# Kernel tuning notes

Measured on AMD Instinct MI355X. Metric: run time of the kernel, lower is better.

The kernel has to match this reference:

```python
import jax, jax.numpy as jnp
from jax import lax
import numpy as np

B, T, NCLS, D = 64, 2048, 20, 2048
LCS_LEN, FSD_LEN = 64, 32
LAMB1, LAMB2, LAMB3 = 1.0, 5e-5, 8e-5
LAMB_LCS, LAMB_FSD = 0.01, 0.01
FEAT_MARGIN = 50.0
THRES = 0.5
GAMMA = 0.1


def cos_sim(a, b):
    a = a / jnp.linalg.norm(a, axis=1, keepdims=True)
    b = b / jnp.linalg.norm(b, axis=1, keepdims=True)
    return a @ b.T


def dp_fsd(c0, c1):
    # soft-LCS/DTW-style recurrence with maxGamma (soft max) over 3 neighbors
    h = c0.shape[-1] // 2
    m = cos_sim(c0[:, :h], c1[:, :h])  # [L, L]
    g = cos_sim(c0[:, h:], c1[:, h:])  # [L, L]
    L = m.shape[0]

    def row_step(prev_row, mg):
        m_row, g_row = mg
        diag = prev_row[:-1]  # C[i-1, j-1]
        up = prev_row[1:]     # C[i-1, j]

        def col_step(left, xs):  # left = C[i, j-1]
            d, u, mij, gij = xs
            neigh = jnp.stack([d, gij + u, gij + left])
            val = mij + GAMMA * jax.nn.logsumexp(neigh / GAMMA)
            return val, val

        _, row_vals = lax.scan(col_step, jnp.zeros((), m.dtype), (diag, up, m_row, g_row))
        new_row = jnp.concatenate([jnp.zeros((1,), m.dtype), row_vals])
        return new_row, None

    final_row, _ = lax.scan(row_step, jnp.zeros(L + 1, m.dtype), (m, g))
    return final_row[-1]


def dp_lcs(c0, c1):
    s = cos_sim(c0, c1)  # [L, L]
    L = s.shape[0]

    def row_step(prev_row, s_row):
        diag = prev_row[:-1]
        up = prev_row[1:]

        def col_step(left, xs):
            d, u, sij = xs
            val = jnp.where(sij > THRES, d + sij, jnp.maximum(u, left))
            return val, val

        _, row_vals = lax.scan(col_step, jnp.zeros((), s.dtype), (diag, up, s_row))
        return jnp.concatenate([jnp.zeros((1,), s.dtype), row_vals]), None

    final_row, _ = lax.scan(row_step, jnp.zeros(L + 1, s.dtype), s)
    return final_row[-1]


def cls_criterion(p, lab):
    return -jnp.mean(jnp.sum(jnp.log(p + 1e-10) * lab, axis=1))


def forward_once(ai_cls, ac_cls, ab_cls, vlab, att, ai_feat, ac_feat, ab_feat, ai_cas):
    bs = ai_cls.shape[0]
    ones = jnp.ones((bs, 1), ai_cls.dtype)
    zeros = jnp.zeros((bs, 1), ai_cls.dtype)
    inst_lab = jnp.concatenate([vlab, zeros], axis=1)
    cont_lab = jnp.concatenate([vlab, ones], axis=1)
    back_lab = jnp.concatenate([jnp.zeros_like(vlab), ones], axis=1)
    inst_lab = inst_lab / jnp.sum(inst_lab, axis=1, keepdims=True)
    cont_lab = cont_lab / jnp.sum(cont_lab, axis=1, keepdims=True)
    back_lab = back_lab / jnp.sum(back_lab, axis=1, keepdims=True)

    inst_loss = cls_criterion(ai_cls, inst_lab)
    cont_loss = cls_criterion(ac_cls, cont_lab)
    back_loss = cls_criterion(ab_cls, back_lab)

    guide_loss = jnp.mean(jnp.sum(jnp.abs(1.0 - ai_cas[:, :, -1] - lax.stop_gradient(att[:, :, 0])), axis=1))

    n_inst = jnp.linalg.norm(ai_feat, axis=1)
    n_cont = jnp.linalg.norm(ac_feat, axis=1)
    n_back = jnp.linalg.norm(ab_feat, axis=1)
    f1 = jnp.maximum(FEAT_MARGIN - n_inst + n_cont, 0.0)
    f2 = jnp.maximum(FEAT_MARGIN - n_cont + n_back, 0.0)
    f3 = n_back
    feat_loss = jnp.mean((f1 + f2 + f3) ** 2)

    sparse_loss = jnp.mean(jnp.sum(att[:, :, :2], axis=1))

    cls_loss = inst_loss + cont_loss + back_loss  # THUMOS14 weights 1/1/1
    return cls_loss + LAMB1 * guide_loss + LAMB2 * feat_loss + LAMB3 * sparse_loss


def _pair_loss(vals, pair_label):
    bs = vals.shape[0]
    pos = jnp.sum(vals * pair_label)
    neg = jnp.sum(vals * (1.0 - pair_label))
    pos_num = jnp.sum(pair_label)
    neg_num = bs - pos_num
    return neg / (neg_num + 1e-10) - pos / (pos_num + 1e-10)


def ftcl_forward(act_inst_cls_0, act_cont_cls_0, act_back_cls_0, vid_label_0, temp_att_0,
                 act_inst_feat_0, act_cont_feat_0, act_back_feat_0, act_inst_cas_0,
                 lcs_candi_0, fsd_act_candi_0, fsd_bak_candi_0,
                 act_inst_cls_1, act_cont_cls_1, act_back_cls_1, vid_label_1, temp_att_1,
                 act_inst_feat_1, act_cont_feat_1, act_back_feat_1, act_inst_cas_1,
                 lcs_candi_1, fsd_act_candi_1, fsd_bak_candi_1):
    loss_0 = forward_once(act_inst_cls_0, act_cont_cls_0, act_back_cls_0, vid_label_0, temp_att_0,
                          act_inst_feat_0, act_cont_feat_0, act_back_feat_0, act_inst_cas_0)
    loss_1 = forward_once(act_inst_cls_1, act_cont_cls_1, act_back_cls_1, vid_label_1, temp_att_1,
                          act_inst_feat_1, act_cont_feat_1, act_back_feat_1, act_inst_cas_1)
    acm_loss = (loss_0 + loss_1) / 2.0

    pair_label = (jnp.sum(vid_label_0 * vid_label_1, axis=1) > 0).astype(jnp.float32)  # [B]

    lcs = jax.vmap(dp_lcs)(lcs_candi_0, lcs_candi_1)  # [B]
    lcs_loss = _pair_loss(lcs, pair_label)

    # pair==1 -> act_1, pair==0 -> bak_1 (matches the per-sample branch in torch)
    fsd_c1 = jnp.where(pair_label[:, None, None] > 0, fsd_act_candi_1, fsd_bak_candi_1)
    fsd = jax.vmap(dp_fsd)(fsd_act_candi_0, fsd_c1)  # [B]
    fsd_loss = _pair_loss(fsd, pair_label)

    return acm_loss + LAMB_LCS * lcs_loss + LAMB_FSD * fsd_loss


def setup_inputs() -> dict:
    key = jax.random.key(0)
    ks = iter(jax.random.split(key, 32))
    rand = lambda s: jax.random.uniform(next(ks), s, jnp.float32)
    randn = lambda s: jax.random.normal(next(ks), s, jnp.float32)
    inp = {}
    for sfx in ('0', '1'):
        inp[f'act_inst_cls_{sfx}'] = rand((B, NCLS + 1))
        inp[f'act_cont_cls_{sfx}'] = rand((B, NCLS + 1))
        inp[f'act_back_cls_{sfx}'] = rand((B, NCLS + 1))
        inp[f'vid_label_{sfx}'] = jnp.ones((B, NCLS), jnp.float32)
        inp[f'temp_att_{sfx}'] = rand((B, T, 3))
        inp[f'act_inst_feat_{sfx}'] = randn((B, D))
        inp[f'act_cont_feat_{sfx}'] = randn((B, D))
        inp[f'act_back_feat_{sfx}'] = randn((B, D))
        inp[f'act_inst_cas_{sfx}'] = rand((B, T, NCLS + 1))
        inp[f'lcs_candi_{sfx}'] = randn((B, LCS_LEN, D))
        inp[f'fsd_act_candi_{sfx}'] = randn((B, FSD_LEN, D))
        inp[f'fsd_bak_candi_{sfx}'] = randn((B, FSD_LEN, D))
    return inp


def reference(act_inst_cls_0, act_cont_cls_0, act_back_cls_0, vid_label_0, temp_att_0,
              act_inst_feat_0, act_cont_feat_0, act_back_feat_0, act_inst_cas_0,
              lcs_candi_0, fsd_act_candi_0, fsd_bak_candi_0,
              act_inst_cls_1, act_cont_cls_1, act_back_cls_1, vid_label_1, temp_att_1,
              act_inst_feat_1, act_cont_feat_1, act_back_feat_1, act_inst_cas_1,
              lcs_candi_1, fsd_act_candi_1, fsd_bak_candi_1):
    return ftcl_forward(act_inst_cls_0, act_cont_cls_0, act_back_cls_0, vid_label_0, temp_att_0,
                        act_inst_feat_0, act_cont_feat_0, act_back_feat_0, act_inst_cas_0,
                        lcs_candi_0, fsd_act_candi_0, fsd_bak_candi_0,
                        act_inst_cls_1, act_cont_cls_1, act_back_cls_1, vid_label_1, temp_att_1,
                        act_inst_feat_1, act_cont_feat_1, act_back_feat_1, act_inst_cas_1,
                        lcs_candi_1, fsd_act_candi_1, fsd_bak_candi_1)
```

## Files before the change

### kernel.cpp

```cpp
#include <hip/hip_runtime.h>
#include <math.h>

#define Bn 64
#define Tn 2048
#define NCLS 20
#define Dn 2048
#define LCSL 64
#define FSDL 32

typedef __bf16 bf16x4 __attribute__((ext_vector_type(4)));
typedef __bf16 bf16x8 __attribute__((ext_vector_type(8)));
typedef float f32x4 __attribute__((ext_vector_type(4)));

#define WS_LCS 0
#define WS_FSD 64
#define WS_NORM 128
#define WS_GS 512
template <int NS>
struct WsOff {
    static constexpr size_t LSQ = 1024;
    static constexpr size_t FSQ = LSQ + (size_t)64 * NS * 128;
    static constexpr size_t SPART = FSQ + (size_t)64 * NS * 64;
    static constexpr size_t MG = SPART + (size_t)64 * NS * 4096;
    static constexpr size_t SC = MG + (size_t)64 * NS * 1024;
    static constexpr size_t PL = SC + 16;
    static constexpr size_t END = PL + 64;
};

#define AUXB 224

template <int NS>
__global__ __launch_bounds__(256) void mega_kernel(
    const float* __restrict__ lcs0, const float* __restrict__ lcs1,
    const float* __restrict__ fA0, const float* __restrict__ fA1,
    const float* __restrict__ fB1,
    const float* __restrict__ vid0, const float* __restrict__ vid1,
    const float* __restrict__ cas0, const float* __restrict__ att0,
    const float* __restrict__ cas1, const float* __restrict__ att1,
    const float* __restrict__ f0, const float* __restrict__ f1,
    const float* __restrict__ f2, const float* __restrict__ f3,
    const float* __restrict__ f4, const float* __restrict__ f5,
    float* __restrict__ ws) {
    constexpr int L = (NS == 16) ? 4 : 3;
    constexpr int KC = 2048 / NS / 64;
    using O = WsOff<NS>;
    __shared__ __align__(16) __bf16 tA[2][4096];
    __shared__ __align__(16) __bf16 tB[2][4096];
    const int t = threadIdx.x;
    const int bid = blockIdx.x;
    const int w = t >> 6, lane = t & 63;
    const int quad = lane >> 4, l16 = lane & 15;

    if (bid < 128) {
        const int gb = bid;
        const int N = Bn * Tn;
        float g0 = 0.f, s0 = 0.f, g1 = 0.f, s1 = 0.f;
        for (int n = gb * 256 + t; n < 2 * N; n += 128 * 256) {
            int sfx = (n >= N);
            int m = sfx ? (n - N) : n;
            const float* cas = sfx ? cas1 : cas0;
            const float* att = sfx ? att1 : att0;
            float a0 = att[m * 3 + 0];
            float a1 = att[m * 3 + 1];
            float g = fabsf(1.0f - cas[m * (NCLS + 1) + NCLS] - a0);
            float s = a0 + a1;
            if (sfx) { g1 += g; s1 += s; } else { g0 += g; s0 += s; }
        }
        float* red = (float*)tA;
        float vals[4] = {g0, s0, g1, s1};
        #pragma unroll
        for (int v = 0; v < 4; ++v) red[v * 256 + t] = vals[v];
        __syncthreads();
        for (int o = 128; o; o >>= 1) {
            if (t < o) {
                #pragma unroll
                for (int v = 0; v < 4; ++v) red[v * 256 + t] += red[v * 256 + t + o];
            }
            __syncthreads();
        }
        if (t < 4) ws[WS_GS + gb * 4 + t] = red[t * 256];
    } else if (bid < AUXB) {
        int R = (bid - 128) * 4 + w;
        const float* arr[6] = {f0, f1, f2, f3, f4, f5};
        const float* p = arr[R >> 6] + (size_t)(R & 63) * Dn;
        float s = 0.f;
        #pragma unroll
        for (int qd = 0; qd < 8; ++qd) {
            float4 v = *(const float4*)(p + qd * 256 + lane * 4);
            s += v.x * v.x + v.y * v.y + v.z * v.z + v.w * v.w;
        }
        for (int off = 32; off; off >>= 1) s += __shfl_down(s, off);
        if (lane == 0) ws[WS_NORM + R] = sqrtf(s);
    } else if (bid < AUXB + 64 * NS) {
        const int gb = bid - AUXB;
        const int b = gb >> L, ks = gb & (NS - 1);
        const float* c0 = lcs0 + (size_t)b * LCSL * Dn + ks * (2048 / NS);
        const float* c1 = lcs1 + (size_t)b * LCSL * Dn + ks * (2048 / NS);

        f32x4 acc[4] = {};
        float sqa[4] = {0.f, 0.f, 0.f, 0.f}, sqb[4] = {0.f, 0.f, 0.f, 0.f};
        float4 pA[4], pB[4];

        auto LOADL = [&](int st) {
            #pragma unroll
            for (int l = 0; l < 4; ++l) {
                int idx4 = l * 256 + t;
                int row = idx4 >> 4, kq4 = idx4 & 15;
                pA[l] = *(const float4*)(c0 + (size_t)row * Dn + st * 64 + kq4 * 4);
                pB[l] = *(const float4*)(c1 + (size_t)row * Dn + st * 64 + kq4 * 4);
            }
        };
        auto WRITEL = [&](int buf) {
            #pragma unroll
            for (int l = 0; l < 4; ++l) {
                int idx4 = l * 256 + t;
                int row = idx4 >> 4, kq4 = idx4 & 15;
                int c = kq4 >> 1, h = kq4 & 1;
                int pos = row * 64 + ((c ^ (row & 7)) << 3) + h * 4;
                float4 av = pA[l], bv = pB[l];
                bf16x4 a4 = {(__bf16)av.x, (__bf16)av.y, (__bf16)av.z, (__bf16)av.w};
                bf16x4 b4 = {(__bf16)bv.x, (__bf16)bv.y, (__bf16)bv.z, (__bf16)bv.w};
                *(bf16x4*)&tA[buf][pos] = a4;
                *(bf16x4*)&tB[buf][pos] = b4;
                sqa[l] += av.x * av.x + av.y * av.y + av.z * av.z + av.w * av.w;
                sqb[l] += bv.x * bv.x + bv.y * bv.y + bv.z * bv.z + bv.w * bv.w;
            }
        };

        LOADL(0);
        WRITEL(0);
        if (KC > 1) LOADL(1);
        __syncthreads();
        for (int kc = 0; kc < KC; ++kc) {
            const int cur = kc & 1;
            #pragma unroll
            for (int s = 0; s < 2; ++s) {
                int ar = w * 16 + l16;
                int ac_ = (s * 4 + quad) ^ (ar & 7);
                bf16x8 af = *(const bf16x8*)&tA[cur][ar * 64 + (ac_ << 3)];
                #pragma unroll
                for (int tj = 0; tj < 4; ++tj) {
                    int br = tj * 16 + l16;
                    int bc = (s * 4 + quad) ^ (br & 7);
                    bf16x8 bf = *(const bf16x8*)&tB[cur][br * 64 + (bc << 3)];
                    acc[tj] = __builtin_amdgcn_mfma_f32_16x16x32_bf16(af, bf, acc[tj], 0, 0, 0);
                }
            }
            if (kc + 1 < KC) {
                WRITEL(cur ^ 1);
                if (kc + 2 < KC) LOADL(kc + 2);
                __syncthreads();
            }
        }
        float* dst = ws + O::SPART + (size_t)(b * NS + ks) * 4096;
        #pragma unroll
        for (int tj = 0; tj < 4; ++tj)
            #pragma unroll
            for (int rg = 0; rg < 4; ++rg)
                dst[(w * 16 + quad * 4 + rg) * 64 + tj * 16 + l16] = acc[tj][rg];
        #pragma unroll
        for (int l = 0; l < 4; ++l) {
            float sa = sqa[l], sb = sqb[l];
            #pragma unroll
            for (int m = 1; m < 16; m <<= 1) {
                sa += __shfl_xor(sa, m);
                sb += __shfl_xor(sb, m);
            }
            if ((t & 15) == 0) {
                int r = l * 16 + (t >> 4);
                float* q = ws + O::LSQ + (size_t)(b * NS + ks) * 128;
                q[r] = sa;
                q[64 + r] = sb;
            }
        }
    } else {
        const int qb = bid - AUXB - 64 * NS;
        const int b = qb >> L;
        const int idx = qb & (NS - 1);
        const int half = idx >> (L - 1);
        const int ks = idx & (NS / 2 - 1);
        float ps = 0.f;
        for (int c = 0; c < NCLS; ++c) ps += vid0[b * NCLS + c] * vid1[b * NCLS + c];
        const float* base1 = (ps > 0.f) ? fA1 : fB1;
        const float* c0 = fA0 + (size_t)b * FSDL * Dn + half * 1024 + ks * (2048 / NS);
        const float* c1 = base1 + (size_t)b * FSDL * Dn + half * 1024 + ks * (2048 / NS);
        const int wi = w >> 1, wj = w & 1;

        f32x4 acc = {};
        float sqa[2] = {0.f, 0.f}, sqb[2] = {0.f, 0.f};
        float4 pA[2], pB[2];

        auto LOADF = [&](int st) {
            #pragma unroll
            for (int l = 0; l < 2; ++l) {
                int idx4 = l * 256 + t;
                int row = idx4 >> 4, kq4 = idx4 & 15;
                pA[l] = *(const float4*)(c0 + (size_t)row * Dn + st * 64 + kq4 * 4);
                pB[l] = *(const float4*)(c1 + (size_t)row * Dn + st * 64 + kq4 * 4);
            }
        };
        auto WRITEF = [&](int buf) {
            #pragma unroll
            for (int l = 0; l < 2; ++l) {
                int idx4 = l * 256 + t;
                int row = idx4 >> 4, kq4 = idx4 & 15;
                int c = kq4 >> 1, h = kq4 & 1;
                int pos = row * 64 + ((c ^ (row & 7)) << 3) + h * 4;
                float4 av = pA[l], bv = pB[l];
                bf16x4 a4 = {(__bf16)av.x, (__bf16)av.y, (__bf16)av.z, (__bf16)av.w};
                bf16x4 b4 = {(__bf16)bv.x, (__bf16)bv.y, (__bf16)bv.z, (__bf16)bv.w};
                *(bf16x4*)&tA[buf][pos] = a4;
                *(bf16x4*)&tB[buf][pos] = b4;
                sqa[l] += av.x * av.x + av.y * av.y + av.z * av.z + av.w * av.w;
                sqb[l] += bv.x * bv.x + bv.y * bv.y + bv.z * bv.z + bv.w * bv.w;
            }
        };

        LOADF(0);
        WRITEF(0);
        if (KC > 1) LOADF(1);
        __syncthreads();
        for (int kc = 0; kc < KC; ++kc) {
            const int cur = kc & 1;
            #pragma unroll
            for (int s = 0; s < 2; ++s) {
                int ar = wi * 16 + l16;
                int ac_ = (s * 4 + quad) ^ (ar & 7);
                bf16x8 af = *(const bf16x8*)&tA[cur][ar * 64 + (ac_ << 3)];
                int br = wj * 16 + l16;
                int bc = (s * 4 + quad) ^ (br & 7);
                bf16x8 bf = *(const bf16x8*)&tB[cur][br * 64 + (bc << 3)];
                acc = __builtin_amdgcn_mfma_f32_16x16x32_bf16(af, bf, acc, 0, 0, 0);
            }
            if (kc + 1 < KC) {
                WRITEF(cur ^ 1);
                if (kc + 2 < KC) LOADF(kc + 2);
                __syncthreads();
            }
        }
        float* dst = ws + O::MG + (size_t)((b * 2 + half) * (NS / 2) + ks) * 1024;
        #pragma unroll
        for (int rg = 0; rg < 4; ++rg)
            dst[(wi * 16 + quad * 4 + rg) * 32 + wj * 16 + l16] = acc[rg];
        #pragma unroll
        for (int l = 0; l < 2; ++l) {
            float sa = sqa[l], sb = sqb[l];
            #pragma unroll
            for (int m = 1; m < 16; m <<= 1) {
                sa += __shfl_xor(sa, m);
                sb += __shfl_xor(sb, m);
            }
            if ((t & 15) == 0) {
                int r = l * 16 + (t >> 4);
                float* qq = ws + O::FSQ + (size_t)((b * 2 + half) * (NS / 2) + ks) * 64;
                qq[r] = sa;
                qq[32 + r] = sb;
            }
        }
    }
}

__device__ __forceinline__ float4 wbr4(float4 v, float4* redw, int t) {
    #pragma unroll
    for (int m = 1; m < 64; m <<= 1) {
        v.x += __shfl_xor(v.x, m);
        v.y += __shfl_xor(v.y, m);
        v.z += __shfl_xor(v.z, m);
        v.w += __shfl_xor(v.w, m);
    }
    if ((t & 63) == 0) redw[t >> 6] = v;
    __syncthreads();
    float4 r;
    r.x = redw[0].x + redw[1].x + redw[2].x + redw[3].x;
    r.y = redw[0].y + redw[1].y + redw[2].y + redw[3].y;
    r.z = redw[0].z + redw[1].z + redw[2].z + redw[3].z;
    r.w = redw[0].w + redw[1].w + redw[2].w + redw[3].w;
    __syncthreads();
    return r;
}

template <int NS>
__global__ __launch_bounds__(256) void dp_kernel(
    float* __restrict__ ws,
    const float* __restrict__ ai0, const float* __restrict__ ac0,
    const float* __restrict__ ab0, const float* __restrict__ vid0,
    const float* __restrict__ ai1, const float* __restrict__ ac1,
    const float* __restrict__ ab1, const float* __restrict__ vid1) {
    using O = WsOff<NS>;
    const int t = threadIdx.x;
    if (blockIdx.x < 64) {
        const int b = blockIdx.x;
        __shared__ float S[64 * 68];
        __shared__ float inv[128];
        if (t < 128) {
            float s = 0.f;
            #pragma unroll
            for (int ks = 0; ks < NS; ++ks)
                s += ws[O::LSQ + (size_t)(b * NS + ks) * 128 + t];
            inv[t] = 1.0f / sqrtf(s);
        }
        __syncthreads();
        const float* sp = ws + O::SPART + (size_t)b * NS * 4096;
        #pragma unroll
        for (int qd = 0; qd < 4; ++qd) {
            int idx4 = qd * 256 + t;
            int i = idx4 >> 4, j = (idx4 & 15) * 4;
            float4 v = {0.f, 0.f, 0.f, 0.f};
            #pragma unroll
            for (int ks = 0; ks < NS; ++ks) {
                float4 p = *(const float4*)(sp + (size_t)ks * 4096 + idx4 * 4);
                v.x += p.x; v.y += p.y; v.z += p.z; v.w += p.w;
            }
            float ri = inv[i];
            S[i * 68 + j + 0] = v.x * ri * inv[64 + j + 0];
            S[i * 68 + j + 1] = v.y * ri * inv[64 + j + 1];
            S[i * 68 + j + 2] = v.z * ri * inv[64 + j + 2];
            S[i * 68 + j + 3] = v.w * ri * inv[64 + j + 3];
        }
        __syncthreads();
        if (t < 64) {
            float prev = 0.f, prevprev = 0.f;
            float sval_next = S[t * 68 + 0];
            for (int d = 2; d <= 128; ++d) {
                float s = sval_next;
                int jn = d - t - 1;
                if (jn >= 0 && jn < 64) sval_next = S[t * 68 + jn];
                float up = __shfl_up(prev, 1);
                float dg = __shfl_up(prevprev, 1);
                if (t == 0) { up = 0.f; dg = 0.f; }
                int j = d - t - 1;
                float left = prev;
                float val = (s > 0.5f) ? (dg + s) : fmaxf(up, left);
                float cur = (j >= 1 && j <= 64) ? val : 0.f;
                prevprev = prev;
                prev = cur;
            }
            if (t == 63) ws[WS_LCS + b] = prev;
        }
    } else if (blockIdx.x < 128) {
        const int b = blockIdx.x - 64;
        __shared__ float M[32 * 36], G[32 * 36];
        __shared__ float inv[128];
        if (t < 128) {
            int half = t >> 6, sub = t & 63;
            float s = 0.f;
            #pragma unroll
            for (int ks = 0; ks < NS / 2; ++ks)
                s += ws[O::FSQ + (size_t)((b * 2 + half) * (NS / 2) + ks) * 64 + sub];
            inv[t] = 1.0f / sqrtf(s);
        }
        __syncthreads();
        {
            int idx4 = t;
            int i = idx4 >> 3, j = (idx4 & 7) * 4;
            float4 vM = {0.f, 0.f, 0.f, 0.f}, vG = {0.f, 0.f, 0.f, 0.f};
            #pragma unroll
            for (int ks = 0; ks < NS / 2; ++ks) {
                float4 pM = *(const float4*)(ws + O::MG + (size_t)((b * 2 + 0) * (NS / 2) + ks) * 1024 + idx4 * 4);
                float4 pG = *(const float4*)(ws + O::MG + (size_t)((b * 2 + 1) * (NS / 2) + ks) * 1024 + idx4 * 4);
                vM.x += pM.x; vM.y += pM.y; vM.z += pM.z; vM.w += pM.w;
                vG.x += pG.x; vG.y += pG.y; vG.z += pG.z; vG.w += pG.w;
            }
            float riM = inv[i], riG = inv[64 + i];
            M[i * 36 + j + 0] = vM.x * riM * inv[32 + j + 0];
            M[i * 36 + j + 1] = vM.y * riM * inv[32 + j + 1];
            M[i * 36 + j + 2] = vM.z * riM * inv[32 + j + 2];
            M[i * 36 + j + 3] = vM.w * riM * inv[32 + j + 3];
            G[i * 36 + j + 0] = vG.x * riG * inv[96 + j + 0];
            G[i * 36 + j + 1] = vG.y * riG * inv[96 + j + 1];
            G[i * 36 + j + 2] = vG.z * riG * inv[96 + j + 2];
            G[i * 36 + j + 3] = vG.w * riG * inv[96 + j + 3];
        }
        __syncthreads();
        if (t < 32) {
            float prev = 0.f, prevprev = 0.f;
            float m_next = M[t * 36 + 0], g_next = G[t * 36 + 0];
            for (int d = 2; d <= 64; ++d) {
                float m = m_next, g = g_next;
                int jn = d - t - 1;
                if (jn >= 0 && jn < 32) { m_next = M[t * 36 + jn]; g_next = G[t * 36 + jn]; }
                float up = __shfl_up(prev, 1);
                float dg = __shfl_up(prevprev, 1);
                if (t == 0) { up = 0.f; dg = 0.f; }
                int j = d - t - 1;
                float left = prev;
                float x0 = dg * 10.0f;
                float x1 = (g + up) * 10.0f;
                float x2 = (g + left) * 10.0f;
                float mx = fmaxf(x0, fmaxf(x1, x2));
                float lse = mx + __logf(__expf(x0 - mx) + __expf(x1 - mx) + __expf(x2 - mx));
                float val = m + 0.1f * lse;
                float cur = (j >= 1 && j <= 32) ? val : 0.f;
                prevprev = prev;
                prev = cur;
            }
            if (t == 31) ws[WS_FSD + b] = prev;
        }
    } else if (blockIdx.x == 128) {
        __shared__ float rs0[Bn], rs1[Bn];
        __shared__ __align__(16) float4 redw[4];
        float plreg = 0.f;
        if (t < Bn) {
            float s0 = 0.f, s1 = 0.f, pp = 0.f;
            for (int c = 0; c < NCLS; ++c) {
                float a = vid0[t * NCLS + c], bl = vid1[t * NCLS + c];
                s0 += a; s1 += bl; pp += a * bl;
            }
            rs0[t] = s0;
            rs1[t] = s1;
            plreg = (pp > 0.f) ? 1.f : 0.f;
            ws[O::PL + t] = plreg;
        }
        __syncthreads();
        float inst0 = 0.f, cont0 = 0.f, back0 = 0.f;
        float inst1 = 0.f, cont1 = 0.f, back1 = 0.f;
        for (int idx = t; idx < Bn * (NCLS + 1); idx += 256) {
            int b = idx / (NCLS + 1), c = idx % (NCLS + 1);
            float v0 = (c < NCLS) ? vid0[b * NCLS + c] : 0.f;
            float v1 = (c < NCLS) ? vid1[b * NCLS + c] : 0.f;
            float wI0 = (c < NCLS) ? (v0 / rs0[b]) : 0.f;
            float wC0 = ((c < NCLS) ? v0 : 1.f) / (rs0[b] + 1.f);
            float wI1 = (c < NCLS) ? (v1 / rs1[b]) : 0.f;
            float wC1 = ((c < NCLS) ? v1 : 1.f) / (rs1[b] + 1.f);
            inst0 += logf(ai0[idx] + 1e-10f) * wI0;
            cont0 += logf(ac0[idx] + 1e-10f) * wC0;
            inst1 += logf(ai1[idx] + 1e-10f) * wI1;
            cont1 += logf(ac1[idx] + 1e-10f) * wC1;
            if (c == NCLS) {
                back0 += logf(ab0[idx] + 1e-10f);
                back1 += logf(ab1[idx] + 1e-10f);
            }
        }
        float4 r1 = wbr4({inst0, cont0, back0, inst1}, redw, t);
        float4 r2 = wbr4({cont1, back1, plreg, 0.f}, redw, t);
        if (t == 0) {
            ws[O::SC + 0] = r1.x; ws[O::SC + 1] = r1.y; ws[O::SC + 2] = r1.z;
            ws[O::SC + 3] = r1.w; ws[O::SC + 4] = r2.x; ws[O::SC + 5] = r2.y;
            ws[O::SC + 12] = r2.z;
        }
    } else if (blockIdx.x == 129) {
        __shared__ __align__(16) float4 redw[4];
        float4 g = {0.f, 0.f, 0.f, 0.f};
        if (t < 128) g = *(const float4*)&ws[WS_GS + t * 4];
        float4 r = wbr4(g, redw, t);
        if (t == 0) {
            ws[O::SC + 6] = r.x; ws[O::SC + 7] = r.y;
            ws[O::SC + 8] = r.z; ws[O::SC + 9] = r.w;
        }
    } else if (blockIdx.x == 130) {
        __shared__ __align__(16) float4 redw[4];
        float fv0 = 0.f, fv1 = 0.f;
        if (t < Bn) {
            const float* nm = ws + WS_NORM;
            {
                float ni = nm[0 * Bn + t], nc = nm[1 * Bn + t], nb = nm[2 * Bn + t];
                float f1 = fmaxf(50.0f - ni + nc, 0.f);
                float f2 = fmaxf(50.0f - nc + nb, 0.f);
                float f = f1 + f2 + nb;
                fv0 = f * f;
            }
            {
                float ni = nm[3 * Bn + t], nc = nm[4 * Bn + t], nb = nm[5 * Bn + t];
                float f1 = fmaxf(50.0f - ni + nc, 0.f);
                float f2 = fmaxf(50.0f - nc + nb, 0.f);
                float f = f1 + f2 + nb;
                fv1 = f * f;
            }
        }
        float4 r = wbr4({fv0, fv1, 0.f, 0.f}, redw, t);
        if (t == 0) {
            ws[O::SC + 10] = r.x; ws[O::SC + 11] = r.y;
        }
    }
}

template <int NS>
__global__ __launch_bounds__(64) void final_kernel(const float* __restrict__ ws,
                                                   float* __restrict__ out) {
    using O = WsOff<NS>;
    const int t = threadIdx.x;
    float pl = ws[O::PL + t];
    float lv = ws[WS_LCS + t];
    float fv = ws[WS_FSD + t];
    float4 v = {lv * pl, lv * (1.f - pl), fv * pl, fv * (1.f - pl)};
    #pragma unroll
    for (int m = 1; m < 64; m <<= 1) {
        v.x += __shfl_xor(v.x, m);
        v.y += __shfl_xor(v.y, m);
        v.z += __shfl_xor(v.z, m);
        v.w += __shfl_xor(v.w, m);
    }
    if (t == 0) {
        const float* sc = ws + O::SC;
        float cls0 = -(sc[0] + sc[1] + sc[2]) / (float)Bn;
        float cls1 = -(sc[3] + sc[4] + sc[5]) / (float)Bn;
        float guide0 = sc[6] / (float)Bn;
        float sparse0 = sc[7] / (float)(Bn * 2);
        float guide1 = sc[8] / (float)Bn;
        float sparse1 = sc[9] / (float)(Bn * 2);
        float sFeat0 = sc[10] / (float)Bn;
        float sFeat1 = sc[11] / (float)Bn;
        float loss0 = cls0 + 1.0f * guide0 + 5e-05f * sFeat0 + 8e-05f * sparse0;
        float loss1 = cls1 + 1.0f * guide1 + 5e-05f * sFeat1 + 8e-05f * sparse1;
        float acm = 0.5f * (loss0 + loss1);
        float posn = sc[12];
        float negn = (float)Bn - posn;
        float lcs_loss = v.y / (negn + 1e-10f) - v.x / (posn + 1e-10f);
        float fsd_loss = v.w / (negn + 1e-10f) - v.z / (posn + 1e-10f);
        out[0] = acm + 0.01f * lcs_loss + 0.01f * fsd_loss;
    }
}

extern "C" void kernel_launch(void* const* d_in, const int* in_sizes, int n_in,
                              void* d_out, int out_size, void* d_ws, size_t ws_size,
                              hipStream_t stream) {
    (void)in_sizes; (void)n_in; (void)out_size;
    const float* ai0  = (const float*)d_in[0];
    const float* ac0  = (const float*)d_in[1];
    const float* ab0  = (const float*)d_in[2];
    const float* vid0 = (const float*)d_in[3];
    const float* att0 = (const float*)d_in[4];
    const float* fi0  = (const float*)d_in[5];
    const float* fc0  = (const float*)d_in[6];
    const float* fb0  = (const float*)d_in[7];
    const float* cas0 = (const float*)d_in[8];
    const float* lcs0 = (const float*)d_in[9];
    const float* fsdA0 = (const float*)d_in[10];
    const float* ai1  = (const float*)d_in[12];
    const float* ac1  = (const float*)d_in[13];
    const float* ab1  = (const float*)d_in[14];
    const float* vid1 = (const float*)d_in[15];
    const float* att1 = (const float*)d_in[16];
    const float* fi1  = (const float*)d_in[17];
    const float* fc1  = (const float*)d_in[18];
    const float* fb1  = (const float*)d_in[19];
    const float* cas1 = (const float*)d_in[20];
    const float* lcs1 = (const float*)d_in[21];
    const float* fsdA1 = (const float*)d_in[22];
    const float* fsdB1 = (const float*)d_in[23];

    float* ws = (float*)d_ws;

    if (ws_size >= WsOff<16>::END * sizeof(float)) {
        mega_kernel<16><<<AUXB + 128 * 16, 256, 0, stream>>>(
            lcs0, lcs1, fsdA0, fsdA1, fsdB1, vid0, vid1, cas0, att0, cas1, att1,
            fi0, fc0, fb0, fi1, fc1, fb1, ws);
        dp_kernel<16><<<131, 256, 0, stream>>>(ws, ai0, ac0, ab0, vid0, ai1, ac1, ab1, vid1);
        final_kernel<16><<<1, 64, 0, stream>>>(ws, (float*)d_out);
    } else {
        mega_kernel<8><<<AUXB + 128 * 8, 256, 0, stream>>>(
            lcs0, lcs1, fsdA0, fsdA1, fsdB1, vid0, vid1, cas0, att0, cas1, att1,
            fi0, fc0, fb0, fi1, fc1, fb1, ws);
        dp_kernel<8><<<131, 256, 0, stream>>>(ws, ai0, ac0, ab0, vid0, ai1, ac1, ab1, vid1);
        final_kernel<8><<<1, 64, 0, stream>>>(ws, (float*)d_out);
    }
}
```

Before: 224.5 us.

## Fuse final reduction into DP kernel via atomic counter and move class loss into mega kernel

Moves the classification-loss block from the DP kernel into an extra block of the mega kernel. The final reduction now runs as a last block of the DP kernel, which spin-waits on an atomic counter cleared by a memset, replacing a separate final kernel launch. It also fixes the split count at 8, widens the DP kernel to 512 threads, and adds a memset call. The spin-wait depends on the waiting block being scheduled alongside the producer blocks.

```diff
diff --git a/kernel.cpp b/kernel.cpp
--- a/kernel.cpp
+++ b/kernel.cpp
@@ -24,241 +24,12 @@
     static constexpr size_t MG = SPART + (size_t)64 * NS * 4096;
     static constexpr size_t SC = MG + (size_t)64 * NS * 1024;
     static constexpr size_t PL = SC + 16;
-    static constexpr size_t END = PL + 64;
+    static constexpr size_t CNT = PL + 64;
+    static constexpr size_t END = CNT + 4;
 };
 
-#define AUXB 224
-
-template <int NS>
-__global__ __launch_bounds__(256) void mega_kernel(
-    const float* __restrict__ lcs0, const float* __restrict__ lcs1,
-    const float* __restrict__ fA0, const float* __restrict__ fA1,
-    const float* __restrict__ fB1,
-    const float* __restrict__ vid0, const float* __restrict__ vid1,
-    const float* __restrict__ cas0, const float* __restrict__ att0,
-    const float* __restrict__ cas1, const float* __restrict__ att1,
-    const float* __restrict__ f0, const float* __restrict__ f1,
-    const float* __restrict__ f2, const float* __restrict__ f3,
-    const float* __restrict__ f4, const float* __restrict__ f5,
-    float* __restrict__ ws) {
-    constexpr int L = (NS == 16) ? 4 : 3;
-    constexpr int KC = 2048 / NS / 64;
-    using O = WsOff<NS>;
-    __shared__ __align__(16) __bf16 tA[2][4096];
-    __shared__ __align__(16) __bf16 tB[2][4096];
-    const int t = threadIdx.x;
-    const int bid = blockIdx.x;
-    const int w = t >> 6, lane = t & 63;
-    const int quad = lane >> 4, l16 = lane & 15;
-
-    if (bid < 128) {
-        const int gb = bid;
-        const int N = Bn * Tn;
-        float g0 = 0.f, s0 = 0.f, g1 = 0.f, s1 = 0.f;
-        for (int n = gb * 256 + t; n < 2 * N; n += 128 * 256) {
-            int sfx = (n >= N);
-            int m = sfx ? (n - N) : n;
-            const float* cas = sfx ? cas1 : cas0;
-            const float* att = sfx ? att1 : att0;
-            float a0 = att[m * 3 + 0];
-            float a1 = att[m * 3 + 1];
-            float g = fabsf(1.0f - cas[m * (NCLS + 1) + NCLS] - a0);
-            float s = a0 + a1;
-            if (sfx) { g1 += g; s1 += s; } else { g0 += g; s0 += s; }
-        }
-        float* red = (float*)tA;
-        float vals[4] = {g0, s0, g1, s1};
-        #pragma unroll
-        for (int v = 0; v < 4; ++v) red[v * 256 + t] = vals[v];
-        __syncthreads();
-        for (int o = 128; o; o >>= 1) {
-            if (t < o) {
-                #pragma unroll
-                for (int v = 0; v < 4; ++v) red[v * 256 + t] += red[v * 256 + t + o];
-            }
-            __syncthreads();
-        }
-        if (t < 4) ws[WS_GS + gb * 4 + t] = red[t * 256];
-    } else if (bid < AUXB) {
-        int R = (bid - 128) * 4 + w;
-        const float* arr[6] = {f0, f1, f2, f3, f4, f5};
-        const float* p = arr[R >> 6] + (size_t)(R & 63) * Dn;
-        float s = 0.f;
-        #pragma unroll
-        for (int qd = 0; qd < 8; ++qd) {
-            float4 v = *(const float4*)(p + qd * 256 + lane * 4);
-            s += v.x * v.x + v.y * v.y + v.z * v.z + v.w * v.w;
-        }
-        for (int off = 32; off; off >>= 1) s += __shfl_down(s, off);
-        if (lane == 0) ws[WS_NORM + R] = sqrtf(s);
-    } else if (bid < AUXB + 64 * NS) {
-        const int gb = bid - AUXB;
-        const int b = gb >> L, ks = gb & (NS - 1);
-        const float* c0 = lcs0 + (size_t)b * LCSL * Dn + ks * (2048 / NS);
-        const float* c1 = lcs1 + (size_t)b * LCSL * Dn + ks * (2048 / NS);
-
-        f32x4 acc[4] = {};
-        float sqa[4] = {0.f, 0.f, 0.f, 0.f}, sqb[4] = {0.f, 0.f, 0.f, 0.f};
-        float4 pA[4], pB[4];
-
-        auto LOADL = [&](int st) {
-            #pragma unroll
-            for (int l = 0; l < 4; ++l) {
-                int idx4 = l * 256 + t;
-                int row = idx4 >> 4, kq4 = idx4 & 15;
-                pA[l] = *(const float4*)(c0 + (size_t)row * Dn + st * 64 + kq4 * 4);
-                pB[l] = *(const float4*)(c1 + (size_t)row * Dn + st * 64 + kq4 * 4);
-            }
-        };
-        auto WRITEL = [&](int buf) {
-            #pragma unroll
-            for (int l = 0; l < 4; ++l) {
-                int idx4 = l * 256 + t;
-                int row = idx4 >> 4, kq4 = idx4 & 15;
-                int c = kq4 >> 1, h = kq4 & 1;
-                int pos = row * 64 + ((c ^ (row & 7)) << 3) + h * 4;
-                float4 av = pA[l], bv = pB[l];
-                bf16x4 a4 = {(__bf16)av.x, (__bf16)av.y, (__bf16)av.z, (__bf16)av.w};
-                bf16x4 b4 = {(__bf16)bv.x, (__bf16)bv.y, (__bf16)bv.z, (__bf16)bv.w};
-                *(bf16x4*)&tA[buf][pos] = a4;
-                *(bf16x4*)&tB[buf][pos] = b4;
-                sqa[l] += av.x * av.x + av.y * av.y + av.z * av.z + av.w * av.w;
-                sqb[l] += bv.x * bv.x + bv.y * bv.y + bv.z * bv.z + bv.w * bv.w;
-            }
-        };
-
-        LOADL(0);
-        WRITEL(0);
-        if (KC > 1) LOADL(1);
-        __syncthreads();
-        for (int kc = 0; kc < KC; ++kc) {
-            const int cur = kc & 1;
-            #pragma unroll
-            for (int s = 0; s < 2; ++s) {
-                int ar = w * 16 + l16;
-                int ac_ = (s * 4 + quad) ^ (ar & 7);
-                bf16x8 af = *(const bf16x8*)&tA[cur][ar * 64 + (ac_ << 3)];
-                #pragma unroll
-                for (int tj = 0; tj < 4; ++tj) {
-                    int br = tj * 16 + l16;
-                    int bc = (s * 4 + quad) ^ (br & 7);
-                    bf16x8 bf = *(const bf16x8*)&tB[cur][br * 64 + (bc << 3)];
-                    acc[tj] = __builtin_amdgcn_mfma_f32_16x16x32_bf16(af, bf, acc[tj], 0, 0, 0);
-                }
-            }
-            if (kc + 1 < KC) {
-                WRITEL(cur ^ 1);
-                if (kc + 2 < KC) LOADL(kc + 2);
-                __syncthreads();
-            }
-        }
-        float* dst = ws + O::SPART + (size_t)(b * NS + ks) * 4096;
-        #pragma unroll
-        for (int tj = 0; tj < 4; ++tj)
-            #pragma unroll
-            for (int rg = 0; rg < 4; ++rg)
-                dst[(w * 16 + quad * 4 + rg) * 64 + tj * 16 + l16] = acc[tj][rg];
-        #pragma unroll
-        for (int l = 0; l < 4; ++l) {
-            float sa = sqa[l], sb = sqb[l];
-            #pragma unroll
-            for (int m = 1; m < 16; m <<= 1) {
-                sa += __shfl_xor(sa, m);
-                sb += __shfl_xor(sb, m);
-            }
-            if ((t & 15) == 0) {
-                int r = l * 16 + (t >> 4);
-                float* q = ws + O::LSQ + (size_t)(b * NS + ks) * 128;
-                q[r] = sa;
-                q[64 + r] = sb;
-            }
-        }
-    } else {
-        const int qb = bid - AUXB - 64 * NS;
-        const int b = qb >> L;
-        const int idx = qb & (NS - 1);
-        const int half = idx >> (L - 1);
-        const int ks = idx & (NS / 2 - 1);
-        float ps = 0.f;
-        for (int c = 0; c < NCLS; ++c) ps += vid0[b * NCLS + c] * vid1[b * NCLS + c];
-        const float* base1 = (ps > 0.f) ? fA1 : fB1;
-        const float* c0 = fA0 + (size_t)b * FSDL * Dn + half * 1024 + ks * (2048 / NS);
-        const float* c1 = base1 + (size_t)b * FSDL * Dn + half * 1024 + ks * (2048 / NS);
-        const int wi = w >> 1, wj = w & 1;
-
-        f32x4 acc = {};
-        float sqa[2] = {0.f, 0.f}, sqb[2] = {0.f, 0.f};
-        float4 pA[2], pB[2];
-
-        auto LOADF = [&](int st) {
-            #pragma unroll
-            for (int l = 0; l < 2; ++l) {
-                int idx4 = l * 256 + t;
-                int row = idx4 >> 4, kq4 = idx4 & 15;
-                pA[l] = *(const float4*)(c0 + (size_t)row * Dn + st * 64 + kq4 * 4);
-                pB[l] = *(const float4*)(c1 + (size_t)row * Dn + st * 64 + kq4 * 4);
-            }
-        };
-        auto WRITEF = [&](int buf) {
-            #pragma unroll
-            for (int l = 0; l < 2; ++l) {
-                int idx4 = l * 256 + t;
-                int row = idx4 >> 4, kq4 = idx4 & 15;
-                int c = kq4 >> 1, h = kq4 & 1;
-                int pos = row * 64 + ((c ^ (row & 7)) << 3) + h * 4;
-                float4 av = pA[l], bv = pB[l];
-                bf16x4 a4 = {(__bf16)av.x, (__bf16)av.y, (__bf16)av.z, (__bf16)av.w};
-                bf16x4 b4 = {(__bf16)bv.x, (__bf16)bv.y, (__bf16)bv.z, (__bf16)bv.w};
-                *(bf16x4*)&tA[buf][pos] = a4;
-                *(bf16x4*)&tB[buf][pos] = b4;
-                sqa[l] += av.x * av.x + av.y * av.y + av.z * av.z + av.w * av.w;
-                sqb[l] += bv.x * bv.x + bv.y * bv.y + bv.z * bv.z + bv.w * bv.w;
-            }
-        };
-
-        LOADF(0);
-        WRITEF(0);
-        if (KC > 1) LOADF(1);
-        __syncthreads();
-        for (int kc = 0; kc < KC; ++kc) {
-            const int cur = kc & 1;
-            #pragma unroll
-            for (int s = 0; s < 2; ++s) {
-                int ar = wi * 16 + l16;
-                int ac_ = (s * 4 + quad) ^ (ar & 7);
-                bf16x8 af = *(const bf16x8*)&tA[cur][ar * 64 + (ac_ << 3)];
-                int br = wj * 16 + l16;
-                int bc = (s * 4 + quad) ^ (br & 7);
-                bf16x8 bf = *(const bf16x8*)&tB[cur][br * 64 + (bc << 3)];
-                acc = __builtin_amdgcn_mfma_f32_16x16x32_bf16(af, bf, acc, 0, 0, 0);
-            }
-            if (kc + 1 < KC) {
-                WRITEF(cur ^ 1);
-                if (kc + 2 < KC) LOADF(kc + 2);
-                __syncthreads();
-            }
-        }
-        float* dst = ws + O::MG + (size_t)((b * 2 + half) * (NS / 2) + ks) * 1024;
-        #pragma unroll
-        for (int rg = 0; rg < 4; ++rg)
-            dst[(wi * 16 + quad * 4 + rg) * 32 + wj * 16 + l16] = acc[rg];
-        #pragma unroll
-        for (int l = 0; l < 2; ++l) {
-            float sa = sqa[l], sb = sqb[l];
-            #pragma unroll
-            for (int m = 1; m < 16; m <<= 1) {
-                sa += __shfl_xor(sa, m);
-                sb += __shfl_xor(sb, m);
-            }
-            if ((t & 15) == 0) {
-                int r = l * 16 + (t >> 4);
-                float* qq = ws + O::FSQ + (size_t)((b * 2 + half) * (NS / 2) + ks) * 64;
-                qq[r] = sa;
-                qq[32 + r] = sb;
-            }
-        }
-    }
-}
+#define NSU 8
+#define AUXB 225
 
 __device__ __forceinline__ float4 wbr4(float4 v, float4* redw, int t) {
     #pragma unroll
@@ -280,13 +51,287 @@
 }
 
 template <int NS>
-__global__ __launch_bounds__(256) void dp_kernel(
-    float* __restrict__ ws,
+__global__ __launch_bounds__(256) void mega_kernel(
+    const float* __restrict__ lcs0, const float* __restrict__ lcs1,
+    const float* __restrict__ fA0, const float* __restrict__ fA1,
+    const float* __restrict__ fB1,
+    const float* __restrict__ vid0, const float* __restrict__ vid1,
+    const float* __restrict__ cas0, const float* __restrict__ att0,
+    const float* __restrict__ cas1, const float* __restrict__ att1,
+    const float* __restrict__ f0, const float* __restrict__ f1,
+    const float* __restrict__ f2, const float* __restrict__ f3,
+    const float* __restrict__ f4, const float* __restrict__ f5,
     const float* __restrict__ ai0, const float* __restrict__ ac0,
-    const float* __restrict__ ab0, const float* __restrict__ vid0,
-    const float* __restrict__ ai1, const float* __restrict__ ac1,
-    const float* __restrict__ ab1, const float* __restrict__ vid1) {
+    const float* __restrict__ ab0, const float* __restrict__ ai1,
+    const float* __restrict__ ac1, const float* __restrict__ ab1,
+    float* __restrict__ ws) {
+    constexpr int L = (NS == 16) ? 4 : 3;
+    constexpr int KC = 2048 / NS / 64;
     using O = WsOff<NS>;
+    __shared__ __align__(16) __bf16 tA[2][4096];
+    __shared__ __align__(16) __bf16 tB[2][4096];
+    const int t = threadIdx.x;
+    const int bid = blockIdx.x;
+    const int w = t >> 6, lane = t & 63;
+    const int quad = lane >> 4, l16 = lane & 15;
+
+    if (bid < 128) {
+        const int gb = bid;
+        const int N = Bn * Tn;
+        float g0 = 0.f, s0 = 0.f, g1 = 0.f, s1 = 0.f;
+        for (int n = gb * 256 + t; n < 2 * N; n += 128 * 256) {
+            int sfx = (n >= N);
+            int m = sfx ? (n - N) : n;
+            const float* cas = sfx ? cas1 : cas0;
+            const float* att = sfx ? att1 : att0;
+            float a0 = att[m * 3 + 0];
+            float a1 = att[m * 3 + 1];
+            float g = fabsf(1.0f - cas[m * (NCLS + 1) + NCLS] - a0);
+            float s = a0 + a1;
+            if (sfx) { g1 += g; s1 += s; } else { g0 += g; s0 += s; }
+        }
+        float* red = (float*)tA;
+        float vals[4] = {g0, s0, g1, s1};
+        #pragma unroll
+        for (int v = 0; v < 4; ++v) red[v * 256 + t] = vals[v];
+        __syncthreads();
+        for (int o = 128; o; o >>= 1) {
+            if (t < o) {
+                #pragma unroll
+                for (int v = 0; v < 4; ++v) red[v * 256 + t] += red[v * 256 + t + o];
+            }
+            __syncthreads();
+        }
+        if (t < 4) ws[WS_GS + gb * 4 + t] = red[t * 256];
+    } else if (bid < 224) {
+        int R = (bid - 128) * 4 + w;
+        const float* arr[6] = {f0, f1, f2, f3, f4, f5};
+        const float* p = arr[R >> 6] + (size_t)(R & 63) * Dn;
+        float s = 0.f;
+        #pragma unroll
+        for (int qd = 0; qd < 8; ++qd) {
+            float4 v = *(const float4*)(p + qd * 256 + lane * 4);
+            s += v.x * v.x + v.y * v.y + v.z * v.z + v.w * v.w;
+        }
+        for (int off = 32; off; off >>= 1) s += __shfl_down(s, off);
+        if (lane == 0) ws[WS_NORM + R] = sqrtf(s);
+    } else if (bid < AUXB) {
+        float* rs0 = (float*)tA;
+        float* rs1 = (float*)tA + 64;
+        float4* redw = (float4*)tB;
+        float plreg = 0.f;
+        if (t < Bn) {
+            float s0 = 0.f, s1 = 0.f, pp = 0.f;
+            for (int c = 0; c < NCLS; ++c) {
+                float a = vid0[t * NCLS + c], bl = vid1[t * NCLS + c];
+                s0 += a; s1 += bl; pp += a * bl;
+            }
+            rs0[t] = s0;
+            rs1[t] = s1;
+            plreg = (pp > 0.f) ? 1.f : 0.f;
+            ws[O::PL + t] = plreg;
+        }
+        __syncthreads();
+        float inst0 = 0.f, cont0 = 0.f, back0 = 0.f;
+        float inst1 = 0.f, cont1 = 0.f, back1 = 0.f;
+        for (int idx = t; idx < Bn * (NCLS + 1); idx += 256) {
+            int b = idx / (NCLS + 1), c = idx % (NCLS + 1);
+            float v0 = (c < NCLS) ? vid0[b * NCLS + c] : 0.f;
+            float v1 = (c < NCLS) ? vid1[b * NCLS + c] : 0.f;
+            float wI0 = (c < NCLS) ? (v0 / rs0[b]) : 0.f;
+            float wC0 = ((c < NCLS) ? v0 : 1.f) / (rs0[b] + 1.f);
+            float wI1 = (c < NCLS) ? (v1 / rs1[b]) : 0.f;
+            float wC1 = ((c < NCLS) ? v1 : 1.f) / (rs1[b] + 1.f);
+            inst0 += logf(ai0[idx] + 1e-10f) * wI0;
+            cont0 += logf(ac0[idx] + 1e-10f) * wC0;
+            inst1 += logf(ai1[idx] + 1e-10f) * wI1;
+            cont1 += logf(ac1[idx] + 1e-10f) * wC1;
+            if (c == NCLS) {
+                back0 += logf(ab0[idx] + 1e-10f);
+                back1 += logf(ab1[idx] + 1e-10f);
+            }
+        }
+        float4 r1 = wbr4({inst0, cont0, back0, inst1}, redw, t);
+        float4 r2 = wbr4({cont1, back1, plreg, 0.f}, redw, t);
+        if (t == 0) {
+            ws[O::SC + 0] = r1.x; ws[O::SC + 1] = r1.y; ws[O::SC + 2] = r1.z;
+            ws[O::SC + 3] = r1.w; ws[O::SC + 4] = r2.x; ws[O::SC + 5] = r2.y;
+            ws[O::SC + 12] = r2.z;
+        }
+    } else if (bid < AUXB + 64 * NS) {
+        const int gb = bid - AUXB;
+        const int b = gb >> L, ks = gb & (NS - 1);
+        const float* c0 = lcs0 + (size_t)b * LCSL * Dn + ks * (2048 / NS);
+        const float* c1 = lcs1 + (size_t)b * LCSL * Dn + ks * (2048 / NS);
+
+        f32x4 acc[4] = {};
+        float sqa[4] = {0.f, 0.f, 0.f, 0.f}, sqb[4] = {0.f, 0.f, 0.f, 0.f};
+        float4 pA[4], pB[4];
+
+        auto LOADL = [&](int st) {
+            #pragma unroll
+            for (int l = 0; l < 4; ++l) {
+                int idx4 = l * 256 + t;
+                int row = idx4 >> 4, kq4 = idx4 & 15;
+                pA[l] = *(const float4*)(c0 + (size_t)row * Dn + st * 64 + kq4 * 4);
+                pB[l] = *(const float4*)(c1 + (size_t)row * Dn + st * 64 + kq4 * 4);
+            }
+        };
+        auto WRITEL = [&](int buf) {
+            #pragma unroll
+            for (int l = 0; l < 4; ++l) {
+                int idx4 = l * 256 + t;
+                int row = idx4 >> 4, kq4 = idx4 & 15;
+                int c = kq4 >> 1, h = kq4 & 1;
+                int pos = row * 64 + ((c ^ (row & 7)) << 3) + h * 4;
+                float4 av = pA[l], bv = pB[l];
+                bf16x4 a4 = {(__bf16)av.x, (__bf16)av.y, (__bf16)av.z, (__bf16)av.w};
+                bf16x4 b4 = {(__bf16)bv.x, (__bf16)bv.y, (__bf16)bv.z, (__bf16)bv.w};
+                *(bf16x4*)&tA[buf][pos] = a4;
+                *(bf16x4*)&tB[buf][pos] = b4;
+                sqa[l] += av.x * av.x + av.y * av.y + av.z * av.z + av.w * av.w;
+                sqb[l] += bv.x * bv.x + bv.y * bv.y + bv.z * bv.z + bv.w * bv.w;
+            }
+        };
+
+        LOADL(0);
+        WRITEL(0);
+        if (KC > 1) LOADL(1);
+        __syncthreads();
+        for (int kc = 0; kc < KC; ++kc) {
+            const int cur = kc & 1;
+            #pragma unroll
+            for (int s = 0; s < 2; ++s) {
+                int ar = w * 16 + l16;
+                int ac_ = (s * 4 + quad) ^ (ar & 7);
+                bf16x8 af = *(const bf16x8*)&tA[cur][ar * 64 + (ac_ << 3)];
+                #pragma unroll
+                for (int tj = 0; tj < 4; ++tj) {
+                    int br = tj * 16 + l16;
+                    int bc = (s * 4 + quad) ^ (br & 7);
+                    bf16x8 bf = *(const bf16x8*)&tB[cur][br * 64 + (bc << 3)];
+                    acc[tj] = __builtin_amdgcn_mfma_f32_16x16x32_bf16(af, bf, acc[tj], 0, 0, 0);
+                }
+            }
+            if (kc + 1 < KC) {
+                WRITEL(cur ^ 1);
+                if (kc + 2 < KC) LOADL(kc + 2);
+                __syncthreads();
+            }
+        }
+        float* dst = ws + O::SPART + (size_t)(b * NS + ks) * 4096;
+        #pragma unroll
+        for (int tj = 0; tj < 4; ++tj)
+            #pragma unroll
+            for (int rg = 0; rg < 4; ++rg)
+                dst[(w * 16 + quad * 4 + rg) * 64 + tj * 16 + l16] = acc[tj][rg];
+        #pragma unroll
+        for (int l = 0; l < 4; ++l) {
+            float sa = sqa[l], sb = sqb[l];
+            #pragma unroll
+            for (int m = 1; m < 16; m <<= 1) {
+                sa += __shfl_xor(sa, m);
+                sb += __shfl_xor(sb, m);
+            }
+            if ((t & 15) == 0) {
+                int r = l * 16 + (t >> 4);
+                float* q = ws + O::LSQ + (size_t)(b * NS + ks) * 128;
+                q[r] = sa;
+                q[64 + r] = sb;
+            }
+        }
+    } else {
+        const int qb = bid - AUXB - 64 * NS;
+        const int b = qb >> L;
+        const int idx = qb & (NS - 1);
+        const int half = idx >> (L - 1);
+        const int ks = idx & (NS / 2 - 1);
+        float ps = 0.f;
+        for (int c = 0; c < NCLS; ++c) ps += vid0[b * NCLS + c] * vid1[b * NCLS + c];
+        const float* base1 = (ps > 0.f) ? fA1 : fB1;
+        const float* c0 = fA0 + (size_t)b * FSDL * Dn + half * 1024 + ks * (2048 / NS);
+        const float* c1 = base1 + (size_t)b * FSDL * Dn + half * 1024 + ks * (2048 / NS);
+        const int wi = w >> 1, wj = w & 1;
+
+        f32x4 acc = {};
+        float sqa[2] = {0.f, 0.f}, sqb[2] = {0.f, 0.f};
+        float4 pA[2], pB[2];
+
+        auto LOADF = [&](int st) {
+            #pragma unroll
+            for (int l = 0; l < 2; ++l) {
+                int idx4 = l * 256 + t;
+                int row = idx4 >> 4, kq4 = idx4 & 15;
+                pA[l] = *(const float4*)(c0 + (size_t)row * Dn + st * 64 + kq4 * 4);
+                pB[l] = *(const float4*)(c1 + (size_t)row * Dn + st * 64 + kq4 * 4);
+            }
+        };
+        auto WRITEF = [&](int buf) {
+            #pragma unroll
+            for (int l = 0; l < 2; ++l) {
+                int idx4 = l * 256 + t;
+                int row = idx4 >> 4, kq4 = idx4 & 15;
+                int c = kq4 >> 1, h = kq4 & 1;
+                int pos = row * 64 + ((c ^ (row & 7)) << 3) + h * 4;
+                float4 av = pA[l], bv = pB[l];
+                bf16x4 a4 = {(__bf16)av.x, (__bf16)av.y, (__bf16)av.z, (__bf16)av.w};
+                bf16x4 b4 = {(__bf16)bv.x, (__bf16)bv.y, (__bf16)bv.z, (__bf16)bv.w};
+                *(bf16x4*)&tA[buf][pos] = a4;
+                *(bf16x4*)&tB[buf][pos] = b4;
+                sqa[l] += av.x * av.x + av.y * av.y + av.z * av.z + av.w * av.w;
+                sqb[l] += bv.x * bv.x + bv.y * bv.y + bv.z * bv.z + bv.w * bv.w;
+            }
+        };
+
+        LOADF(0);
+        WRITEF(0);
+        if (KC > 1) LOADF(1);
+        __syncthreads();
+        for (int kc = 0; kc < KC; ++kc) {
+            const int cur = kc & 1;
+            #pragma unroll
+            for (int s = 0; s < 2; ++s) {
+                int ar = wi * 16 + l16;
+                int ac_ = (s * 4 + quad) ^ (ar & 7);
+                bf16x8 af = *(const bf16x8*)&tA[cur][ar * 64 + (ac_ << 3)];
+                int br = wj * 16 + l16;
+                int bc = (s * 4 + quad) ^ (br & 7);
+                bf16x8 bf = *(const bf16x8*)&tB[cur][br * 64 + (bc << 3)];
+                acc = __builtin_amdgcn_mfma_f32_16x16x32_bf16(af, bf, acc, 0, 0, 0);
+            }
+            if (kc + 1 < KC) {
+                WRITEF(cur ^ 1);
+                if (kc + 2 < KC) LOADF(kc + 2);
+                __syncthreads();
+            }
+        }
+        float* dst = ws + O::MG + (size_t)((b * 2 + half) * (NS / 2) + ks) * 1024;
+        #pragma unroll
+        for (int rg = 0; rg < 4; ++rg)
+            dst[(wi * 16 + quad * 4 + rg) * 32 + wj * 16 + l16] = acc[rg];
+        #pragma unroll
+        for (int l = 0; l < 2; ++l) {
+            float sa = sqa[l], sb = sqb[l];
+            #pragma unroll
+            for (int m = 1; m < 16; m <<= 1) {
+                sa += __shfl_xor(sa, m);
+                sb += __shfl_xor(sb, m);
+            }
+            if ((t & 15) == 0) {
+                int r = l * 16 + (t >> 4);
+                float* qq = ws + O::FSQ + (size_t)((b * 2 + half) * (NS / 2) + ks) * 64;
+                qq[r] = sa;
+                qq[32 + r] = sb;
+            }
+        }
+    }
+}
+
+template <int NS>
+__global__ __launch_bounds__(512) void dp_kernel(float* __restrict__ ws,
+                                                 float* __restrict__ out) {
+    using O = WsOff<NS>;
+    unsigned* cnt = (unsigned*)(ws + O::CNT);
     const int t = threadIdx.x;
     if (blockIdx.x < 64) {
         const int b = blockIdx.x;
@@ -302,8 +347,8 @@
         __syncthreads();
         const float* sp = ws + O::SPART + (size_t)b * NS * 4096;
         #pragma unroll
-        for (int qd = 0; qd < 4; ++qd) {
-            int idx4 = qd * 256 + t;
+        for (int qd = 0; qd < 2; ++qd) {
+            int idx4 = qd * 512 + t;
             int i = idx4 >> 4, j = (idx4 & 15) * 4;
             float4 v = {0.f, 0.f, 0.f, 0.f};
             #pragma unroll
@@ -337,6 +382,9 @@
             }
             if (t == 63) ws[WS_LCS + b] = prev;
         }
+        __threadfence();
+        __syncthreads();
+        if (t == 0) atomicAdd(cnt, 1u);
     } else if (blockIdx.x < 128) {
         const int b = blockIdx.x - 64;
         __shared__ float M[32 * 36], G[32 * 36];
@@ -350,7 +398,7 @@
             inv[t] = 1.0f / sqrtf(s);
         }
         __syncthreads();
-        {
+        if (t < 256) {
             int idx4 = t;
             int i = idx4 >> 3, j = (idx4 & 7) * 4;
             float4 vM = {0.f, 0.f, 0.f, 0.f}, vG = {0.f, 0.f, 0.f, 0.f};
@@ -396,62 +444,32 @@
             }
             if (t == 31) ws[WS_FSD + b] = prev;
         }
+        __threadfence();
+        __syncthreads();
+        if (t == 0) atomicAdd(cnt, 1u);
     } else if (blockIdx.x == 128) {
-        __shared__ float rs0[Bn], rs1[Bn];
-        __shared__ __align__(16) float4 redw[4];
-        float plreg = 0.f;
-        if (t < Bn) {
-            float s0 = 0.f, s1 = 0.f, pp = 0.f;
-            for (int c = 0; c < NCLS; ++c) {
-                float a = vid0[t * NCLS + c], bl = vid1[t * NCLS + c];
-                s0 += a; s1 += bl; pp += a * bl;
-            }
-            rs0[t] = s0;
-            rs1[t] = s1;
-            plreg = (pp > 0.f) ? 1.f : 0.f;
-            ws[O::PL + t] = plreg;
-        }
-        __syncthreads();
-        float inst0 = 0.f, cont0 = 0.f, back0 = 0.f;
-        float inst1 = 0.f, cont1 = 0.f, back1 = 0.f;
-        for (int idx = t; idx < Bn * (NCLS + 1); idx += 256) {
-            int b = idx / (NCLS + 1), c = idx % (NCLS + 1);
-            float v0 = (c < NCLS) ? vid0[b * NCLS + c] : 0.f;
-            float v1 = (c < NCLS) ? vid1[b * NCLS + c] : 0.f;
-            float wI0 = (c < NCLS) ? (v0 / rs0[b]) : 0.f;
-            float wC0 = ((c < NCLS) ? v0 : 1.f) / (rs0[b] + 1.f);
-            float wI1 = (c < NCLS) ? (v1 / rs1[b]) : 0.f;
-            float wC1 = ((c < NCLS) ? v1 : 1.f) / (rs1[b] + 1.f);
-            inst0 += logf(ai0[idx] + 1e-10f) * wI0;
-            cont0 += logf(ac0[idx] + 1e-10f) * wC0;
-            inst1 += logf(ai1[idx] + 1e-10f) * wI1;
-            cont1 += logf(ac1[idx] + 1e-10f) * wC1;
-            if (c == NCLS) {
-                back0 += logf(ab0[idx] + 1e-10f);
-                back1 += logf(ab1[idx] + 1e-10f);
-            }
-        }
-        float4 r1 = wbr4({inst0, cont0, back0, inst1}, redw, t);
-        float4 r2 = wbr4({cont1, back1, plreg, 0.f}, redw, t);
-        if (t == 0) {
-            ws[O::SC + 0] = r1.x; ws[O::SC + 1] = r1.y; ws[O::SC + 2] = r1.z;
-            ws[O::SC + 3] = r1.w; ws[O::SC + 4] = r2.x; ws[O::SC + 5] = r2.y;
-            ws[O::SC + 12] = r2.z;
-        }
+        if (t < 64) {
+            float4 a = *(const float4*)&ws[WS_GS + t * 4];
+            float4 b2 = *(const float4*)&ws[WS_GS + (t + 64) * 4];
+            a.x += b2.x; a.y += b2.y; a.z += b2.z; a.w += b2.w;
+            #pragma unroll
+            for (int m = 1; m < 64; m <<= 1) {
+                a.x += __shfl_xor(a.x, m);
+                a.y += __shfl_xor(a.y, m);
+                a.z += __shfl_xor(a.z, m);
+                a.w += __shfl_xor(a.w, m);
+            }
+            if (t == 0) {
+                ws[O::SC + 6] = a.x; ws[O::SC + 7] = a.y;
+                ws[O::SC + 8] = a.z; ws[O::SC + 9] = a.w;
+            }
+        }
+        __threadfence();
+        if (t == 0) atomicAdd(cnt, 1u);
     } else if (blockIdx.x == 129) {
-        __shared__ __align__(16) float4 redw[4];
-        float4 g = {0.f, 0.f, 0.f, 0.f};
-        if (t < 128) g = *(const float4*)&ws[WS_GS + t * 4];
-        float4 r = wbr4(g, redw, t);
-        if (t == 0) {
-            ws[O::SC + 6] = r.x; ws[O::SC + 7] = r.y;
-            ws[O::SC + 8] = r.z; ws[O::SC + 9] = r.w;
-        }
-    } else if (blockIdx.x == 130) {
-        __shared__ __align__(16) float4 redw[4];
-        float fv0 = 0.f, fv1 = 0.f;
-        if (t < Bn) {
+        if (t < 64) {
             const float* nm = ws + WS_NORM;
+            float fv0, fv1;
             {
                 float ni = nm[0 * Bn + t], nc = nm[1 * Bn + t], nb = nm[2 * Bn + t];
                 float f1 = fmaxf(50.0f - ni + nc, 0.f);
@@ -466,55 +484,62 @@
                 float f = f1 + f2 + nb;
                 fv1 = f * f;
             }
-        }
-        float4 r = wbr4({fv0, fv1, 0.f, 0.f}, redw, t);
+            #pragma unroll
+            for (int m = 1; m < 64; m <<= 1) {
+                fv0 += __shfl_xor(fv0, m);
+                fv1 += __shfl_xor(fv1, m);
+            }
+            if (t == 0) {
+                ws[O::SC + 10] = fv0; ws[O::SC + 11] = fv1;
+            }
+        }
+        __threadfence();
+        if (t == 0) atomicAdd(cnt, 1u);
+    } else {
         if (t == 0) {
-            ws[O::SC + 10] = r.x; ws[O::SC + 11] = r.y;
-        }
-    }
-}
-
-template <int NS>
-__global__ __launch_bounds__(64) void final_kernel(const float* __restrict__ ws,
-                                                   float* __restrict__ out) {
-    using O = WsOff<NS>;
-    const int t = threadIdx.x;
-    float pl = ws[O::PL + t];
-    float lv = ws[WS_LCS + t];
-    float fv = ws[WS_FSD + t];
-    float4 v = {lv * pl, lv * (1.f - pl), fv * pl, fv * (1.f - pl)};
-    #pragma unroll
-    for (int m = 1; m < 64; m <<= 1) {
-        v.x += __shfl_xor(v.x, m);
-        v.y += __shfl_xor(v.y, m);
-        v.z += __shfl_xor(v.z, m);
-        v.w += __shfl_xor(v.w, m);
-    }
-    if (t == 0) {
-        const float* sc = ws + O::SC;
-        float cls0 = -(sc[0] + sc[1] + sc[2]) / (float)Bn;
-        float cls1 = -(sc[3] + sc[4] + sc[5]) / (float)Bn;
-        float guide0 = sc[6] / (float)Bn;
-        float sparse0 = sc[7] / (float)(Bn * 2);
-        float guide1 = sc[8] / (float)Bn;
-        float sparse1 = sc[9] / (float)(Bn * 2);
-        float sFeat0 = sc[10] / (float)Bn;
-        float sFeat1 = sc[11] / (float)Bn;
-        float loss0 = cls0 + 1.0f * guide0 + 5e-05f * sFeat0 + 8e-05f * sparse0;
-        float loss1 = cls1 + 1.0f * guide1 + 5e-05f * sFeat1 + 8e-05f * sparse1;
-        float acm = 0.5f * (loss0 + loss1);
-        float posn = sc[12];
-        float negn = (float)Bn - posn;
-        float lcs_loss = v.y / (negn + 1e-10f) - v.x / (posn + 1e-10f);
-        float fsd_loss = v.w / (negn + 1e-10f) - v.z / (posn + 1e-10f);
-        out[0] = acm + 0.01f * lcs_loss + 0.01f * fsd_loss;
+            while (atomicAdd(cnt, 0u) < 130u) __builtin_amdgcn_s_sleep(8);
+        }
+        __syncthreads();
+        __threadfence();
+        if (t < 64) {
+            float pl = ws[O::PL + t];
+            float lv = ws[WS_LCS + t];
+            float fv = ws[WS_FSD + t];
+            float4 v = {lv * pl, lv * (1.f - pl), fv * pl, fv * (1.f - pl)};
+            #pragma unroll
+            for (int m = 1; m < 64; m <<= 1) {
+                v.x += __shfl_xor(v.x, m);
+                v.y += __shfl_xor(v.y, m);
+                v.z += __shfl_xor(v.z, m);
+                v.w += __shfl_xor(v.w, m);
+            }
+            if (t == 0) {
+                const float* sc = ws + O::SC;
+                float cls0 = -(sc[0] + sc[1] + sc[2]) / (float)Bn;
+                float cls1 = -(sc[3] + sc[4] + sc[5]) / (float)Bn;
+                float guide0 = sc[6] / (float)Bn;
+                float sparse0 = sc[7] / (float)(Bn * 2);
+                float guide1 = sc[8] / (float)Bn;
+                float sparse1 = sc[9] / (float)(Bn * 2);
+                float sFeat0 = sc[10] / (float)Bn;
+                float sFeat1 = sc[11] / (float)Bn;
+                float loss0 = cls0 + 1.0f * guide0 + 5e-05f * sFeat0 + 8e-05f * sparse0;
+                float loss1 = cls1 + 1.0f * guide1 + 5e-05f * sFeat1 + 8e-05f * sparse1;
+                float acm = 0.5f * (loss0 + loss1);
+                float posn = sc[12];
+                float negn = (float)Bn - posn;
+                float lcs_loss = v.y / (negn + 1e-10f) - v.x / (posn + 1e-10f);
+                float fsd_loss = v.w / (negn + 1e-10f) - v.z / (posn + 1e-10f);
+                out[0] = acm + 0.01f * lcs_loss + 0.01f * fsd_loss;
+            }
+        }
     }
 }
 
 extern "C" void kernel_launch(void* const* d_in, const int* in_sizes, int n_in,
                               void* d_out, int out_size, void* d_ws, size_t ws_size,
                               hipStream_t stream) {
-    (void)in_sizes; (void)n_in; (void)out_size;
+    (void)in_sizes; (void)n_in; (void)out_size; (void)ws_size;
     const float* ai0  = (const float*)d_in[0];
     const float* ac0  = (const float*)d_in[1];
     const float* ab0  = (const float*)d_in[2];
@@ -541,17 +566,10 @@
 
     float* ws = (float*)d_ws;
 
-    if (ws_size >= WsOff<16>::END * sizeof(float)) {
-        mega_kernel<16><<<AUXB + 128 * 16, 256, 0, stream>>>(
-            lcs0, lcs1, fsdA0, fsdA1, fsdB1, vid0, vid1, cas0, att0, cas1, att1,
-            fi0, fc0, fb0, fi1, fc1, fb1, ws);
-        dp_kernel<16><<<131, 256, 0, stream>>>(ws, ai0, ac0, ab0, vid0, ai1, ac1, ab1, vid1);
-        final_kernel<16><<<1, 64, 0, stream>>>(ws, (float*)d_out);
-    } else {
-        mega_kernel<8><<<AUXB + 128 * 8, 256, 0, stream>>>(
-            lcs0, lcs1, fsdA0, fsdA1, fsdB1, vid0, vid1, cas0, att0, cas1, att1,
-            fi0, fc0, fb0, fi1, fc1, fb1, ws);
-        dp_kernel<8><<<131, 256, 0, stream>>>(ws, ai0, ac0, ab0, vid0, ai1, ac1, ab1, vid1);
-        final_kernel<8><<<1, 64, 0, stream>>>(ws, (float*)d_out);
-    }
+    hipMemsetAsync((char*)d_ws + WsOff<NSU>::CNT * sizeof(float), 0, sizeof(unsigned), stream);
+
+    mega_kernel<NSU><<<AUXB + 128 * NSU, 256, 0, stream>>>(
+        lcs0, lcs1, fsdA0, fsdA1, fsdB1, vid0, vid1, cas0, att0, cas1, att1,
+        fi0, fc0, fb0, fi1, fc1, fb1, ai0, ac0, ab0, ai1, ac1, ab1, ws);
+    dp_kernel<NSU><<<131, 512, 0, stream>>>(ws, (float*)d_out);
 }
```

New measurement: 231.6 us. 3.1% more time.
